# Performance work log

Hardware: AMD Instinct MI355X
Metric: run time of the kernel (lower is better)

## Reference

```python
import jax, jax.numpy as jnp
import numpy as np
from math import factorial

# ---- module hyperparameters (from init_kwargs) ----
SPECIES = np.array([1, 6, 7, 8], np.int32)
LOW, HIGH, NG, RSWITCH, W, LMAX = 0.0, 6.0, 20, 1.0, 2.0, 2
LWEIGHTS = np.array([1.0, 1.0, 1.0], np.float32)
INVF = [2.0, 2.0, 2.0]


def _angular_tables():
    comps, weights, idx, inv = [], [], [], []
    for i in range(LMAX + 1):
        for k in range(i + 1):
            for m in range(i - k + 1):
                n = i - k - m
                comps.append([n, m, k])
                weights.append(factorial(i) / (factorial(n) * factorial(m) * factorial(k)))
                idx.append(i)
                inv.append(INVF[i])
    return (np.array(comps, np.int32), np.array(weights, np.float32),
            np.array(idx, np.int32), np.array(inv, np.float32))

COMPS, ANGW, ANGIDX, INVFACT = _angular_tables()   # 10 angular components for lmax=2
OFFSETS = np.linspace(LOW, HIGH, NG + 1, dtype=np.float32)[1:]
SQRTPI = np.float32(np.sqrt(np.pi))
NSP = len(SPECIES)
COMBOS = [(i, j) for i in range(NSP) for j in range(i + 1, NSP)]
NMBODY = NSP + len(COMBOS)
FPSIZE = NG * (LMAX + 1) * NMBODY


def _int_pow(x, e):
    # e in {0,1,2}; avoids NaN from pow(negative_base, float_exponent)
    return jnp.where(e == 0, jnp.ones_like(x), jnp.where(e == 1, x, x * x))


def _forward(coordinates, nuclear_charges, natom_counts, neighbours):
    B, N, _ = coordinates.shape
    mask = neighbours >= 0                              # padded slots are -1
    nb = jnp.maximum(neighbours, 0)                     # safe_fill
    bidx = jnp.arange(B)[:, None, None]
    local = coordinates[bidx, nb]                       # [B,N,M,3] neighbour gather
    nbh = coordinates[:, :, None, :] - local
    nbh = jnp.where(mask[..., None], nbh, 1.0)          # keep padded slots finite
    d = jnp.linalg.norm(nbh, axis=3)                    # [B,N,M]
    coeff = mask.astype(coordinates.dtype)
    nbr_z = nuclear_charges[bidx, nb]                   # [B,N,M]

    dsw = (d - RSWITCH) / (HIGH - RSWITCH)
    cut = 1.0 - 6.0 * dsw**5 + 15.0 * dsw**4 - 10.0 * dsw**3
    d2 = d * d
    sigma2 = jnp.log(1.0 + W / d2)
    mu = jnp.log(d / jnp.sqrt(1.0 + W / d2))
    off = jnp.asarray(OFFSETS)
    centered = (jnp.log(off) - mu[..., None]) ** 2      # [B,N,M,G]
    s2 = sigma2[..., None]
    radial = (1.0 / (off * jnp.sqrt(s2) * SQRTPI)) * jnp.exp(-centered / (2.0 * s2)) \
             * cut[..., None] * coeff[..., None]        # [B,N,M,G]

    expo = jnp.asarray(INVFACT + ANGIDX.astype(np.float32))
    inv_scaling = (1.0 / d[..., None]) ** expo * coeff[..., None]   # [B,N,M,A]
    comps = jnp.asarray(COMPS)
    angular = inv_scaling \
        * _int_pow(nbh[..., None, 0], comps[:, 0]) \
        * _int_pow(nbh[..., None, 1], comps[:, 1]) \
        * _int_pow(nbh[..., None, 2], comps[:, 2])      # [B,N,M,A]

    angw = jnp.asarray(ANGW)
    lw = jnp.asarray(LWEIGHTS)
    onehot = jnp.asarray((ANGIDX[:, None] == np.arange(LMAX + 1)[None, :]).astype(np.float32))

    sp_masks = [(nbr_z == int(z)).astype(coordinates.dtype) for z in SPECIES]

    def group_fp(gmask):
        ang = angular * gmask[..., None]
        t = jnp.einsum('bnma,bnmg->bnag', ang, radial)          # sum over neighbours
        orb = angw[None, None, :, None] * (t * t)               # [B,N,A,G]
        elem = jnp.einsum('bnag,al->bnlg', orb, onehot)         # index_add over l
        return lw[None, None, :, None] * elem                   # [B,N,L+1,G]

    fps = [group_fp(m) for m in sp_masks]
    for (i, j) in COMBOS:
        gmask = jnp.maximum(sp_masks[i], sp_masks[j])
        fps.append(group_fp(gmask) - (fps[i] + fps[j]))

    fp = jnp.stack(fps, axis=3)                                 # [B,N,L+1,NMBODY,G]
    atom_mask = (jnp.arange(N)[None, :] < natom_counts[:, None]).astype(coordinates.dtype)
    fp = fp * atom_mask[:, :, None, None, None]
    return fp.reshape(B, N, FPSIZE)


def setup_inputs() -> dict:
    rng = np.random.default_rng(0)
    B, N, M = 128, 128, 64
    box = 13.5
    coords = rng.uniform(0.0, box, (B, N, 3)).astype(np.float32)
    charges = rng.choice(np.array([1, 6, 7, 8], np.int32), size=(B, N)).astype(np.int32)
    counts = rng.integers(96, N + 1, B).astype(np.int32)
    diff = coords[:, :, None, :] - coords[:, None, :, :]
    dist = np.linalg.norm(diff, axis=-1)
    exist = np.arange(N)[None, :] < counts[:, None]
    valid = (dist < HIGH) & (dist > 1e-6) & exist[:, :, None] & exist[:, None, :]
    order = np.argsort(~valid, axis=2, kind='stable')[:, :, :M]
    vmask = np.take_along_axis(valid, order, axis=2)
    neighbours = np.where(vmask, order, -1).astype(np.int32)
    return {
        "coordinates": jnp.asarray(coords),
        "nuclear_charges": jnp.asarray(charges),
        "natom_counts": jnp.asarray(counts),
        "neighbours": jnp.asarray(neighbours),
    }


def reference(coordinates, nuclear_charges, natom_counts, neighbours):
    return _forward(coordinates, nuclear_charges, natom_counts, neighbours)
```

## Files before the change

### kernel.cpp

```cpp
#include <hip/hip_runtime.h>


#define B_   128
#define N_   128
#define M_   64
#define NG_  20
#define NSP_ 4
#define FPSIZE_ 600
#define APB  16
#define NTASK (APB * M_)
#define BLOCK_THREADS (APB * NG_)
#define P1ITER 4

__global__ __launch_bounds__(BLOCK_THREADS)
void gto_fp_kernel(const float* __restrict__ coords,
                   const int*   __restrict__ charges,
                   const int*   __restrict__ counts,
                   const int*   __restrict__ neigh,
                   float*       __restrict__ out)
{
    __shared__ float4 sP[APB][M_ + 1];
    __shared__ float2 sQ[APB][M_ + 1];
    __shared__ int s_cnt[APB][NSP_];
    __shared__ int s_start[APB][NSP_];
    __shared__ int s_pos[APB][NSP_];

    const int tid = threadIdx.x;
    const int blockBase = blockIdx.x * APB;
    const int bidx = blockBase / N_;

    if (tid < APB * NSP_) ((int*)s_cnt)[tid] = 0;
    __syncthreads();

    float4 rP[P1ITER];
    float2 rQ[P1ITER];
    int    rls[P1ITER];
    bool   rv[P1ITER];

#pragma unroll
    for (int it = 0; it < P1ITER; ++it) {
        const int t = tid + it * BLOCK_THREADS;
        bool v = (t < NTASK);
        int la = 0, s = 0;
        float4 P = make_float4(0.f, 0.f, 0.f, 0.f);
        float2 Q = make_float2(0.f, 0.f);
        if (v) {
            la = t >> 6;
            const int m  = t & 63;
            const int atom = blockBase + la;
            const int nb = neigh[atom * M_ + m];
            if (nb < 0) {
                v = false;
            } else {
                const int nidx = bidx * N_ + nb;
                const float dx = coords[atom * 3 + 0] - coords[nidx * 3 + 0];
                const float dy = coords[atom * 3 + 1] - coords[nidx * 3 + 1];
                const float dz = coords[atom * 3 + 2] - coords[nidx * 3 + 2];
                const int   z  = charges[nidx];

                const float d2     = dx * dx + dy * dy + dz * dz;
                const float inv_d  = __builtin_amdgcn_rsqf(d2);
                const float d      = d2 * inv_d;
                const float inv_d2 = inv_d * inv_d;

                const float dsw  = (d - 1.0f) * 0.2f;
                const float dsw2 = dsw * dsw;
                const float cut  = 1.0f - dsw2 * dsw * fmaf(6.0f, dsw2, fmaf(-15.0f, dsw, 10.0f));

                const float sigma2 = __logf(fmaf(2.0f, inv_d2, 1.0f));
                const float mu     = 0.5f * (__logf(d2) - sigma2);
                const float amp    = fmaxf(__builtin_amdgcn_rsqf(sigma2) * cut * inv_d2,
                                           1.0e-30f);

                const float F  = -0.72134752f * __builtin_amdgcn_rcpf(sigma2);
                const float Fm = F * mu;
                const float c0 = F;
                const float c1 = -(Fm + Fm);
                const float c2 = fmaf(Fm, mu, __log2f(amp));

                s = (z == 1) ? 0 : (z - 5);
                P = make_float4(c0, c1, c2, dx * inv_d);
                Q = make_float2(dy * inv_d, dz * inv_d);
                atomicAdd(&s_cnt[la][s], 1);
            }
        }
        rP[it] = P; rQ[it] = Q; rls[it] = (la << 2) | s; rv[it] = v;
    }
    __syncthreads();

    if (tid < APB) {
        const int c0 = s_cnt[tid][0], c1 = s_cnt[tid][1], c2 = s_cnt[tid][2];
        s_start[tid][0] = 0;            s_pos[tid][0] = 0;
        s_start[tid][1] = c0;           s_pos[tid][1] = c0;
        s_start[tid][2] = c0 + c1;      s_pos[tid][2] = c0 + c1;
        s_start[tid][3] = c0 + c1 + c2; s_pos[tid][3] = c0 + c1 + c2;
    }
    __syncthreads();

#pragma unroll
    for (int it = 0; it < P1ITER; ++it) {
        if (rv[it]) {
            const int la = rls[it] >> 2, s = rls[it] & 3;
            const int slot = atomicAdd(&s_pos[la][s], 1);
            sP[la][slot] = rP[it];
            sQ[la][slot] = rQ[it];
        }
    }
    __syncthreads();

    const int g  = tid % NG_;
    const int la = tid / NG_;
    const int atom = blockBase + la;
    const int n = atom % N_;

    const float off         = 0.3f * (float)(g + 1);
    const float lo          = __logf(off);
    const float lo2         = lo * lo;
    const float inv_off_spi = 1.0f / (off * 1.7724538509055159f);

    float T[NSP_][10];
#pragma unroll
    for (int s = 0; s < NSP_; ++s)
#pragma unroll
        for (int a = 0; a < 10; ++a) T[s][a] = 0.0f;

#define BODY(SS, P, Q)                                                        \
    {                                                                         \
        const float rad = __builtin_amdgcn_exp2f(                             \
            fmaf(P.x, lo2, fmaf(P.y, lo, P.z)));                              \
        const float rx = rad * P.w, ry = rad * Q.x, rz = rad * Q.y;           \
        T[SS][0] += rad;                                                      \
        T[SS][1] += rx;  T[SS][2] += ry;  T[SS][3] += rz;                     \
        T[SS][4] = fmaf(rx, P.w, T[SS][4]);                                   \
        T[SS][5] = fmaf(rx, Q.x, T[SS][5]);                                   \
        T[SS][6] = fmaf(ry, Q.x, T[SS][6]);                                   \
        T[SS][7] = fmaf(rx, Q.y, T[SS][7]);                                   \
        T[SS][8] = fmaf(ry, Q.y, T[SS][8]);                                   \
        T[SS][9] = fmaf(rz, Q.y, T[SS][9]);                                   \
    }

#define ACC(SS)                                                               \
    {                                                                         \
        const int e0 = s_start[la][SS];                                       \
        const int e1 = e0 + s_cnt[la][SS];                                    \
        int m = e0;                                                           \
        for (; m + 1 < e1; m += 2) {                                          \
            const float4 Pa = sP[la][m];     const float2 Qa = sQ[la][m];     \
            const float4 Pb = sP[la][m + 1]; const float2 Qb = sQ[la][m + 1]; \
            BODY(SS, Pa, Qa)                                                  \
            BODY(SS, Pb, Qb)                                                  \
        }                                                                     \
        if (m < e1) {                                                         \
            const float4 Pa = sP[la][m]; const float2 Qa = sQ[la][m];         \
            BODY(SS, Pa, Qa)                                                  \
        }                                                                     \
    }
    ACC(0) ACC(1) ACC(2) ACC(3)
#undef ACC
#undef BODY

    const float amask = (n < counts[bidx]) ? 1.0f : 0.0f;
    const float scale = amask * inv_off_spi * inv_off_spi;
    float* op = out + atom * FPSIZE_ + g;

#pragma unroll
    for (int l = 0; l < 3; ++l) {
        const int a0 = (l == 0) ? 0 : (l == 1) ? 1 : 4;
        const int a1 = (l == 0) ? 1 : (l == 1) ? 4 : 10;
#pragma unroll
        for (int s = 0; s < NSP_; ++s) {
            float v = 0.0f;
#pragma unroll
            for (int a = a0; a < a1; ++a) {
                const float w = (a == 5 || a == 7 || a == 8) ? 2.0f : 1.0f;
                v = fmaf(w * T[s][a], T[s][a], v);
            }
            op[(l * 10 + s) * NG_] = scale * v;
        }
        int mb = 4;
#pragma unroll
        for (int i = 0; i < NSP_; ++i) {
#pragma unroll
            for (int j = i + 1; j < NSP_; ++j) {
                float v = 0.0f;
#pragma unroll
                for (int a = a0; a < a1; ++a) {
                    const float w = (a == 5 || a == 7 || a == 8) ? 2.0f : 1.0f;
                    v = fmaf(w * T[i][a], T[j][a], v);
                }
                op[(l * 10 + mb) * NG_] = scale * (2.0f * v);
                ++mb;
            }
        }
    }
}

extern "C" void kernel_launch(void* const* d_in, const int* in_sizes, int n_in,
                              void* d_out, int out_size, void* d_ws, size_t ws_size,
                              hipStream_t stream) {
    const float* coords  = (const float*)d_in[0];
    const int*   charges = (const int*)d_in[1];
    const int*   counts  = (const int*)d_in[2];
    const int*   neigh   = (const int*)d_in[3];
    float*       outp    = (float*)d_out;

    const int blocks = (B_ * N_) / APB;
    gto_fp_kernel<<<blocks, BLOCK_THREADS, 0, stream>>>(coords, charges, counts, neigh, outp);
}
```

Before: 84.61 us.

## Process two Gaussian offsets per thread and double atoms per block

Each thread now accumulates two Gaussian grid points, so it reads each staged neighbour from shared memory once for both and writes float2 outputs. The block handles 32 atoms with 320 threads. Phase one is split into a counting pass and a compute-and-scatter pass, so per-thread register arrays are no longer held across a barrier, at the cost of reading the neighbour indices twice. Doubling the accumulator arrays (80 floats) raises register pressure, and there are half as many blocks, which may lower occupancy.

```diff
diff --git a/kernel.cpp b/kernel.cpp
--- a/kernel.cpp
+++ b/kernel.cpp
@@ -7,10 +7,9 @@
 #define NG_  20
 #define NSP_ 4
 #define FPSIZE_ 600
-#define APB  16
+#define APB  32
 #define NTASK (APB * M_)
-#define BLOCK_THREADS (APB * NG_)
-#define P1ITER 4
+#define BLOCK_THREADS 320
 
 __global__ __launch_bounds__(BLOCK_THREADS)
 void gto_fp_kernel(const float* __restrict__ coords,
@@ -32,59 +31,14 @@
     if (tid < APB * NSP_) ((int*)s_cnt)[tid] = 0;
     __syncthreads();
 
-    float4 rP[P1ITER];
-    float2 rQ[P1ITER];
-    int    rls[P1ITER];
-    bool   rv[P1ITER];
-
-#pragma unroll
-    for (int it = 0; it < P1ITER; ++it) {
-        const int t = tid + it * BLOCK_THREADS;
-        bool v = (t < NTASK);
-        int la = 0, s = 0;
-        float4 P = make_float4(0.f, 0.f, 0.f, 0.f);
-        float2 Q = make_float2(0.f, 0.f);
-        if (v) {
-            la = t >> 6;
-            const int m  = t & 63;
-            const int atom = blockBase + la;
-            const int nb = neigh[atom * M_ + m];
-            if (nb < 0) {
-                v = false;
-            } else {
-                const int nidx = bidx * N_ + nb;
-                const float dx = coords[atom * 3 + 0] - coords[nidx * 3 + 0];
-                const float dy = coords[atom * 3 + 1] - coords[nidx * 3 + 1];
-                const float dz = coords[atom * 3 + 2] - coords[nidx * 3 + 2];
-                const int   z  = charges[nidx];
-
-                const float d2     = dx * dx + dy * dy + dz * dz;
-                const float inv_d  = __builtin_amdgcn_rsqf(d2);
-                const float d      = d2 * inv_d;
-                const float inv_d2 = inv_d * inv_d;
-
-                const float dsw  = (d - 1.0f) * 0.2f;
-                const float dsw2 = dsw * dsw;
-                const float cut  = 1.0f - dsw2 * dsw * fmaf(6.0f, dsw2, fmaf(-15.0f, dsw, 10.0f));
-
-                const float sigma2 = __logf(fmaf(2.0f, inv_d2, 1.0f));
-                const float mu     = 0.5f * (__logf(d2) - sigma2);
-                const float amp    = fmaxf(__builtin_amdgcn_rsqf(sigma2) * cut * inv_d2,
-                                           1.0e-30f);
-
-                const float F  = -0.72134752f * __builtin_amdgcn_rcpf(sigma2);
-                const float Fm = F * mu;
-                const float c0 = F;
-                const float c1 = -(Fm + Fm);
-                const float c2 = fmaf(Fm, mu, __log2f(amp));
-
-                s = (z == 1) ? 0 : (z - 5);
-                P = make_float4(c0, c1, c2, dx * inv_d);
-                Q = make_float2(dy * inv_d, dz * inv_d);
-                atomicAdd(&s_cnt[la][s], 1);
-            }
+    for (int t = tid; t < NTASK; t += BLOCK_THREADS) {
+        const int la = t >> 6, m = t & 63;
+        const int nb = neigh[(blockBase + la) * M_ + m];
+        if (nb >= 0) {
+            const int z = charges[bidx * N_ + nb];
+            const int s = (z == 1) ? 0 : (z - 5);
+            atomicAdd(&s_cnt[la][s], 1);
         }
-        rP[it] = P; rQ[it] = Q; rls[it] = (la << 2) | s; rv[it] = v;
     }
     __syncthreads();
 
@@ -97,46 +51,82 @@
     }
     __syncthreads();
 
-#pragma unroll
-    for (int it = 0; it < P1ITER; ++it) {
-        if (rv[it]) {
-            const int la = rls[it] >> 2, s = rls[it] & 3;
-            const int slot = atomicAdd(&s_pos[la][s], 1);
-            sP[la][slot] = rP[it];
-            sQ[la][slot] = rQ[it];
-        }
-    }
-    __syncthreads();
-
-    const int g  = tid % NG_;
-    const int la = tid / NG_;
+    for (int t = tid; t < NTASK; t += BLOCK_THREADS) {
+        const int la = t >> 6, m = t & 63;
+        const int atom = blockBase + la;
+        const int nb = neigh[atom * M_ + m];
+        if (nb < 0) continue;
+        const int nidx = bidx * N_ + nb;
+        const float dx = coords[atom * 3 + 0] - coords[nidx * 3 + 0];
+        const float dy = coords[atom * 3 + 1] - coords[nidx * 3 + 1];
+        const float dz = coords[atom * 3 + 2] - coords[nidx * 3 + 2];
+        const int   z  = charges[nidx];
+
+        const float d2     = dx * dx + dy * dy + dz * dz;
+        const float inv_d  = __builtin_amdgcn_rsqf(d2);
+        const float d      = d2 * inv_d;
+        const float inv_d2 = inv_d * inv_d;
+
+        const float dsw  = (d - 1.0f) * 0.2f;
+        const float dsw2 = dsw * dsw;
+        const float cut  = 1.0f - dsw2 * dsw * fmaf(6.0f, dsw2, fmaf(-15.0f, dsw, 10.0f));
+
+        const float sigma2 = __logf(fmaf(2.0f, inv_d2, 1.0f));
+        const float mu     = 0.5f * (__logf(d2) - sigma2);
+        const float amp    = fmaxf(__builtin_amdgcn_rsqf(sigma2) * cut * inv_d2,
+                                   1.0e-30f);
+
+        const float F  = -0.72134752f * __builtin_amdgcn_rcpf(sigma2);
+        const float Fm = F * mu;
+        const float c2 = fmaf(Fm, mu, __log2f(amp));
+
+        const int s = (z == 1) ? 0 : (z - 5);
+        const int slot = atomicAdd(&s_pos[la][s], 1);
+        sP[la][slot] = make_float4(F, -(Fm + Fm), c2, dx * inv_d);
+        sQ[la][slot] = make_float2(dy * inv_d, dz * inv_d);
+    }
+    __syncthreads();
+
+    const int la = tid / 10;
+    const int u  = tid - la * 10;
     const int atom = blockBase + la;
-    const int n = atom % N_;
-
-    const float off         = 0.3f * (float)(g + 1);
-    const float lo          = __logf(off);
-    const float lo2         = lo * lo;
-    const float inv_off_spi = 1.0f / (off * 1.7724538509055159f);
-
-    float T[NSP_][10];
+    const int g0 = 2 * u;
+
+    const float off0 = 0.3f * (float)(g0 + 1);
+    const float off1 = 0.3f * (float)(g0 + 2);
+    const float lo0 = __logf(off0), lo1 = __logf(off1);
+    const float q0 = lo0 * lo0,     q1 = lo1 * lo1;
+
+    float T0[NSP_][10], T1[NSP_][10];
 #pragma unroll
     for (int s = 0; s < NSP_; ++s)
 #pragma unroll
-        for (int a = 0; a < 10; ++a) T[s][a] = 0.0f;
+        for (int a = 0; a < 10; ++a) { T0[s][a] = 0.0f; T1[s][a] = 0.0f; }
 
 #define BODY(SS, P, Q)                                                        \
     {                                                                         \
-        const float rad = __builtin_amdgcn_exp2f(                             \
-            fmaf(P.x, lo2, fmaf(P.y, lo, P.z)));                              \
-        const float rx = rad * P.w, ry = rad * Q.x, rz = rad * Q.y;           \
-        T[SS][0] += rad;                                                      \
-        T[SS][1] += rx;  T[SS][2] += ry;  T[SS][3] += rz;                     \
-        T[SS][4] = fmaf(rx, P.w, T[SS][4]);                                   \
-        T[SS][5] = fmaf(rx, Q.x, T[SS][5]);                                   \
-        T[SS][6] = fmaf(ry, Q.x, T[SS][6]);                                   \
-        T[SS][7] = fmaf(rx, Q.y, T[SS][7]);                                   \
-        T[SS][8] = fmaf(ry, Q.y, T[SS][8]);                                   \
-        T[SS][9] = fmaf(rz, Q.y, T[SS][9]);                                   \
+        const float ea = fmaf(P.x, q0, fmaf(P.y, lo0, P.z));                  \
+        const float eb = fmaf(P.x, q1, fmaf(P.y, lo1, P.z));                  \
+        const float ra = __builtin_amdgcn_exp2f(ea);                          \
+        const float rb = __builtin_amdgcn_exp2f(eb);                          \
+        const float rax = ra * P.w, ray = ra * Q.x, raz = ra * Q.y;           \
+        const float rbx = rb * P.w, rby = rb * Q.x, rbz = rb * Q.y;           \
+        T0[SS][0] += ra;                                                      \
+        T0[SS][1] += rax; T0[SS][2] += ray; T0[SS][3] += raz;                 \
+        T0[SS][4] = fmaf(rax, P.w, T0[SS][4]);                                \
+        T0[SS][5] = fmaf(rax, Q.x, T0[SS][5]);                                \
+        T0[SS][6] = fmaf(ray, Q.x, T0[SS][6]);                                \
+        T0[SS][7] = fmaf(rax, Q.y, T0[SS][7]);                                \
+        T0[SS][8] = fmaf(ray, Q.y, T0[SS][8]);                                \
+        T0[SS][9] = fmaf(raz, Q.y, T0[SS][9]);                                \
+        T1[SS][0] += rb;                                                      \
+        T1[SS][1] += rbx; T1[SS][2] += rby; T1[SS][3] += rbz;                 \
+        T1[SS][4] = fmaf(rbx, P.w, T1[SS][4]);                                \
+        T1[SS][5] = fmaf(rbx, Q.x, T1[SS][5]);                                \
+        T1[SS][6] = fmaf(rby, Q.x, T1[SS][6]);                                \
+        T1[SS][7] = fmaf(rbx, Q.y, T1[SS][7]);                                \
+        T1[SS][8] = fmaf(rby, Q.y, T1[SS][8]);                                \
+        T1[SS][9] = fmaf(rbz, Q.y, T1[SS][9]);                                \
     }
 
 #define ACC(SS)                                                               \
@@ -159,9 +149,13 @@
 #undef ACC
 #undef BODY
 
+    const int n = atom & (N_ - 1);
     const float amask = (n < counts[bidx]) ? 1.0f : 0.0f;
-    const float scale = amask * inv_off_spi * inv_off_spi;
-    float* op = out + atom * FPSIZE_ + g;
+    const float is0 = 1.0f / (off0 * 1.7724538509055159f);
+    const float is1 = 1.0f / (off1 * 1.7724538509055159f);
+    const float sc0 = amask * is0 * is0;
+    const float sc1 = amask * is1 * is1;
+    float* op = out + atom * FPSIZE_ + g0;
 
 #pragma unroll
     for (int l = 0; l < 3; ++l) {
@@ -169,26 +163,29 @@
         const int a1 = (l == 0) ? 1 : (l == 1) ? 4 : 10;
 #pragma unroll
         for (int s = 0; s < NSP_; ++s) {
-            float v = 0.0f;
+            float v0 = 0.0f, v1 = 0.0f;
 #pragma unroll
             for (int a = a0; a < a1; ++a) {
                 const float w = (a == 5 || a == 7 || a == 8) ? 2.0f : 1.0f;
-                v = fmaf(w * T[s][a], T[s][a], v);
+                v0 = fmaf(w * T0[s][a], T0[s][a], v0);
+                v1 = fmaf(w * T1[s][a], T1[s][a], v1);
             }
-            op[(l * 10 + s) * NG_] = scale * v;
+            *(float2*)(op + (l * 10 + s) * NG_) = make_float2(sc0 * v0, sc1 * v1);
         }
         int mb = 4;
 #pragma unroll
         for (int i = 0; i < NSP_; ++i) {
 #pragma unroll
             for (int j = i + 1; j < NSP_; ++j) {
-                float v = 0.0f;
+                float v0 = 0.0f, v1 = 0.0f;
 #pragma unroll
                 for (int a = a0; a < a1; ++a) {
                     const float w = (a == 5 || a == 7 || a == 8) ? 2.0f : 1.0f;
-                    v = fmaf(w * T[i][a], T[j][a], v);
+                    v0 = fmaf(w * T0[i][a], T0[j][a], v0);
+                    v1 = fmaf(w * T1[i][a], T1[j][a], v1);
                 }
-                op[(l * 10 + mb) * NG_] = scale * (2.0f * v);
+                *(float2*)(op + (l * 10 + mb) * NG_) =
+                    make_float2(sc0 * (2.0f * v0), sc1 * (2.0f * v1));
                 ++mb;
             }
         }
```

Result: no change. 85.77 us (+1.4%).
